# Kernel tuning notes

Measured on AMD Instinct MI355X. Metric: run time of the kernel, lower is better.

## Reference

```python
import jax, jax.numpy as jnp
import numpy as np

CLIP = 5.0  # clip_value from init


def setup_inputs() -> dict:
    key = jax.random.key(0)
    ks = jax.random.split(key, 6)
    B, T, I, H = 128, 1024, 256, 512
    s = 1.0 / np.sqrt(H)
    return {
        "x": jax.random.normal(ks[0], (B, T, I), dtype=jnp.float32),
        "h0": jax.random.normal(ks[1], (1, H), dtype=jnp.float32),
        "w_ih": jax.random.normal(ks[2], (3 * H, I), dtype=jnp.float32) * s,
        "w_hh": jax.random.normal(ks[3], (3 * H, H), dtype=jnp.float32) * s,
        "b_ih": jax.random.normal(ks[4], (3 * H,), dtype=jnp.float32) * s,
        "b_hh": jax.random.normal(ks[5], (3 * H,), dtype=jnp.float32) * s,
    }


def reference(x, h0, w_ih, w_hh, b_ih, b_hh):
    # x: [B, T, I], h0: [1, H]
    B = x.shape[0]
    h_init = jnp.tile(h0, (B, 1))  # [B, H]
    # Precompute all input projections in one big GEMM: [T, B, 3H]
    gi_all = jnp.einsum('bti,gi->tbg', x, w_ih) + b_ih

    def step(h, gi):
        gh = h @ w_hh.T + b_hh                      # [B, 3H]
        ir, iz, inn = jnp.split(gi, 3, axis=-1)
        hr, hz, hn = jnp.split(gh, 3, axis=-1)
        r = jax.nn.sigmoid(ir + hr)
        z = jax.nn.sigmoid(iz + hz)
        n = jnp.tanh(inn + r * hn)
        h_new = (1.0 - z) * n + z * h
        h_new = jnp.clip(h_new, -CLIP, CLIP)
        return h_new, h_new

    h_last, out = jax.lax.scan(step, h_init, gi_all)  # out: [T, B, H]
    output = jnp.transpose(out, (1, 0, 2))            # [B, T, H]
    return output, h_last
```

## Files before the change

kernel.cpp:

```cpp
#include <hip/hip_runtime.h>
#include <math.h>

#define T_SEQ 1024
#define B_SZ  128
#define I_SZ  256
#define H_SZ  512
#define G_SZ  1536

#define NBS   8
#define MB    16
#define NHS   16
#define HB    32
#define GB    96
#define NTHR  384
#define PGB   384

typedef _Float16 f16;
typedef _Float16 half8 __attribute__((ext_vector_type(8)));
typedef _Float16 f16x4 __attribute__((ext_vector_type(4)));
typedef float f32x4 __attribute__((ext_vector_type(4)));

__device__ __forceinline__ f32x4 load_f4_cohere_nw(const void* p) {
    f32x4 v;
    asm volatile("global_load_dwordx4 %0, %1, off sc0 sc1" : "=v"(v) : "v"(p));
    return v;
}
__device__ __forceinline__ f16x4 load_f16x4_nw(const void* p) {
    f16x4 v;
    asm volatile("global_load_dwordx2 %0, %1, off" : "=v"(v) : "v"(p));
    return v;
}
__device__ __forceinline__ unsigned load_u32_cohere(const void* p) {
    unsigned v;
    asm volatile("global_load_dword %0, %1, off sc0 sc1\n\ts_waitcnt vmcnt(0)"
                 : "=v"(v) : "v"(p) : "memory");
    return v;
}
__device__ __forceinline__ void store_u32_cohere(void* p, unsigned v) {
    asm volatile("global_store_dword %0, %1, off sc0 sc1"
                 :: "v"(p), "v"(v) : "memory");
}
__device__ __forceinline__ void wait_vm0() {
    asm volatile("s_waitcnt vmcnt(0)" ::: "memory");
    __builtin_amdgcn_sched_barrier(0);
}
__device__ __forceinline__ void wait_vm1() {
    asm volatile("s_waitcnt vmcnt(1)" ::: "memory");
    __builtin_amdgcn_sched_barrier(0);
}

__global__ void setup_kernel(const float* __restrict__ w_ih,
                             const float* __restrict__ w_hh,
                             const float* __restrict__ h0,
                             f16* __restrict__ wp16,
                             f16* __restrict__ wf16,
                             f16* __restrict__ hbuf0,
                             unsigned int* __restrict__ flags) {
    const int i0 = blockIdx.x * blockDim.x + threadIdx.x;
    const int stride = gridDim.x * blockDim.x;
    for (int i = i0; i < I_SZ * G_SZ; i += stride)
        wp16[i] = (f16)w_ih[i];
    for (int i = i0; i < NHS * GB * H_SZ; i += stride) {
        int hs  = i / (GB * H_SZ);
        int rem = i % (GB * H_SZ);
        int gl = rem / H_SZ, k = rem % H_SZ;
        int gate = gl >> 5, c = gl & 31;
        int gg = gate * H_SZ + hs * HB + c;
        wf16[i] = (f16)w_hh[(size_t)gg * H_SZ + k];
    }
    for (int i = i0; i < B_SZ * H_SZ; i += stride)
        hbuf0[i] = (f16)h0[i % H_SZ];
    if (i0 < NBS * NHS * 16) flags[i0] = 0;
}

__global__ __launch_bounds__(512, 1)
void proj_kernel(const float* __restrict__ x,
                 const f16* __restrict__ wp16,
                 const float* __restrict__ b_ih,
                 f16* __restrict__ gi16) {
    const int t  = blockIdx.x >> 2;
    const int g0 = (blockIdx.x & 3) * PGB;
    const int tid  = threadIdx.x;
    const int wid  = tid >> 6;
    const int lane = tid & 63;
    const int col  = lane & 15;
    const int krow = lane >> 4;

    __shared__ __align__(16) unsigned char x_lds[128 * 512];

    #pragma unroll
    for (int j = 0; j < 8; ++j) {
        int idx = tid + j * 512;
        int b = idx >> 5, k16 = idx & 31;
        const float* xp = x + ((size_t)b * T_SEQ + t) * I_SZ + k16 * 8;
        float4 v0 = *reinterpret_cast<const float4*>(xp);
        float4 v1 = *reinterpret_cast<const float4*>(xp + 4);
        half8 hv;
        hv[0] = (f16)v0.x; hv[1] = (f16)v0.y; hv[2] = (f16)v0.z; hv[3] = (f16)v0.w;
        hv[4] = (f16)v1.x; hv[5] = (f16)v1.y; hv[6] = (f16)v1.z; hv[7] = (f16)v1.w;
        unsigned addr = ((unsigned)(b * 512 + k16 * 16)) ^ (((unsigned)(b & 7)) << 4);
        *reinterpret_cast<half8*>(x_lds + addr) = hv;
    }

    const int gw0 = g0 + wid * 48;
    half8 af[3][8];
    #pragma unroll
    for (int m = 0; m < 3; ++m)
        #pragma unroll
        for (int k = 0; k < 8; ++k)
            af[m][k] = *reinterpret_cast<const half8*>(
                wp16 + (size_t)(gw0 + m * 16 + col) * I_SZ + k * 32 + krow * 8);

    float bias[3][4];
    #pragma unroll
    for (int m = 0; m < 3; ++m)
        #pragma unroll
        for (int r = 0; r < 4; ++r)
            bias[m][r] = b_ih[gw0 + m * 16 + krow * 4 + r];

    __syncthreads();

    #pragma unroll
    for (int nt = 0; nt < 8; ++nt) {
        const int b0 = nt * 16;
        f32x4 acc0 = {0.f,0.f,0.f,0.f}, acc1 = {0.f,0.f,0.f,0.f}, acc2 = {0.f,0.f,0.f,0.f};
        const int brow = b0 + col;
        const unsigned bswz = ((unsigned)(brow & 7)) << 4;
        #pragma unroll
        for (int k = 0; k < 8; ++k) {
            half8 bf = *reinterpret_cast<const half8*>(
                x_lds + (((unsigned)(brow * 512 + k * 64 + krow * 16)) ^ bswz));
            acc0 = __builtin_amdgcn_mfma_f32_16x16x32_f16(af[0][k], bf, acc0, 0, 0, 0);
            acc1 = __builtin_amdgcn_mfma_f32_16x16x32_f16(af[1][k], bf, acc1, 0, 0, 0);
            acc2 = __builtin_amdgcn_mfma_f32_16x16x32_f16(af[2][k], bf, acc2, 0, 0, 0);
        }
        #pragma unroll
        for (int r = 0; r < 4; ++r) {
            int gr = gw0 + krow * 4 + r;
            gi16[((size_t)t * G_SZ + gr)      * B_SZ + brow] = (f16)(acc0[r] + bias[0][r]);
            gi16[((size_t)t * G_SZ + gr + 16) * B_SZ + brow] = (f16)(acc1[r] + bias[1][r]);
            gi16[((size_t)t * G_SZ + gr + 32) * B_SZ + brow] = (f16)(acc2[r] + bias[2][r]);
        }
    }
}

__global__ __launch_bounds__(NTHR, 1)
void gru_persist(const f16* __restrict__ gi,
                 const f16* __restrict__ wf16,
                 const float* __restrict__ h0,
                 const float* __restrict__ b_hh,
                 f16* __restrict__ hbuf0,
                 f16* __restrict__ hbuf1,
                 unsigned int* __restrict__ flags,
                 float* __restrict__ out) {
    const int bs  = blockIdx.x & (NBS - 1);
    const int hs  = blockIdx.x >> 3;
    const int tid = threadIdx.x;

    __shared__ __align__(16) unsigned char h_lds[MB * H_SZ * 2];
    __shared__ float act_r[MB][HB + 1];
    __shared__ float act_z[MB][HB + 1];
    __shared__ float act_n[MB][HB + 1];
    __shared__ float act_i[MB][HB + 1];

    const int wid  = tid >> 6;
    const int lane = tid & 63;
    const int gate = wid >> 1;
    const int sub  = wid & 1;
    const int col  = lane & 15;
    const int krow = lane >> 4;
    const int c_local = sub * 16 + col;
    const int g_glob  = gate * H_SZ + hs * HB + c_local;

    half8 bfrag[16];
    {
        const f16* wp = wf16 + ((size_t)hs * GB + gate * HB + c_local) * H_SZ
                             + krow * 8;
        #pragma unroll
        for (int kk = 0; kk < 16; ++kk)
            bfrag[kk] = *reinterpret_cast<const half8*>(wp + kk * 32);
    }
    const float bias = b_hh[g_glob];

    const int cb = tid >> 4;
    const int cc = (tid & 15) * 2;
    float hm0 = 0.f, hm1 = 0.f;
    if (tid < 256) { hm0 = h0[hs * HB + cc]; hm1 = h0[hs * HB + cc + 1]; }

    const unsigned a_base = (unsigned)(col * 1024 + krow * 16);
    const unsigned a_swz  = ((unsigned)(col & 7)) << 4;

    unsigned int* myflag = flags + (size_t)(bs * NHS + hs) * 16;

    for (int t = 0; t < T_SEQ; ++t) {
        const f16* hin = (t & 1) ? hbuf1 : hbuf0;
        f16*      hout = (t & 1) ? hbuf0 : hbuf1;

        const int i0 = tid, i1 = tid + NTHR, i2 = tid + 2 * NTHR;
        f32x4 hv0 = load_f4_cohere_nw(
            hin + (size_t)(bs * MB + (i0 >> 6)) * H_SZ + (i0 & 63) * 8);
        f32x4 hv1 = load_f4_cohere_nw(
            hin + (size_t)(bs * MB + (i1 >> 6)) * H_SZ + (i1 & 63) * 8);
        f32x4 hv2;
        if (i2 < 1024)
            hv2 = load_f4_cohere_nw(
                hin + (size_t)(bs * MB + (i2 >> 6)) * H_SZ + (i2 & 63) * 8);
        f16x4 gv = load_f16x4_nw(
            gi + ((size_t)t * G_SZ + g_glob) * B_SZ + bs * MB + krow * 4);
        wait_vm1();

        {
            unsigned a0 = ((unsigned)((i0 >> 6) * 1024 + (i0 & 63) * 16))
                          ^ (((unsigned)((i0 >> 6) & 7)) << 4);
            *reinterpret_cast<f32x4*>(h_lds + a0) = hv0;
            unsigned a1 = ((unsigned)((i1 >> 6) * 1024 + (i1 & 63) * 16))
                          ^ (((unsigned)((i1 >> 6) & 7)) << 4);
            *reinterpret_cast<f32x4*>(h_lds + a1) = hv1;
            if (i2 < 1024) {
                unsigned a2 = ((unsigned)((i2 >> 6) * 1024 + (i2 & 63) * 16))
                              ^ (((unsigned)((i2 >> 6) & 7)) << 4);
                *reinterpret_cast<f32x4*>(h_lds + a2) = hv2;
            }
        }
        __syncthreads();

        f32x4 acc = {0.f, 0.f, 0.f, 0.f};
        #pragma unroll
        for (int kk = 0; kk < 16; ++kk) {
            half8 av = *reinterpret_cast<const half8*>(
                h_lds + ((a_base + kk * 64) ^ a_swz));
            acc = __builtin_amdgcn_mfma_f32_16x16x32_f16(av, bfrag[kk], acc, 0, 0, 0);
        }
        wait_vm0();

        if (gate == 0) {
            #pragma unroll
            for (int r = 0; r < 4; ++r)
                act_r[krow * 4 + r][c_local] =
                    1.f / (1.f + __expf(-(acc[r] + bias + (float)gv[r])));
        } else if (gate == 1) {
            #pragma unroll
            for (int r = 0; r < 4; ++r)
                act_z[krow * 4 + r][c_local] =
                    1.f / (1.f + __expf(-(acc[r] + bias + (float)gv[r])));
        } else {
            #pragma unroll
            for (int r = 0; r < 4; ++r) {
                act_n[krow * 4 + r][c_local] = acc[r] + bias;
                act_i[krow * 4 + r][c_local] = (float)gv[r];
            }
        }
        __syncthreads();

        if (tid < 256) {
            float r0 = act_r[cb][cc],     r1 = act_r[cb][cc + 1];
            float z0 = act_z[cb][cc],     z1 = act_z[cb][cc + 1];
            float a0 = act_i[cb][cc]     + r0 * act_n[cb][cc];
            float a1 = act_i[cb][cc + 1] + r1 * act_n[cb][cc + 1];
            float n0 = 1.f - 2.f / (__expf(2.f * a0) + 1.f);
            float n1 = 1.f - 2.f / (__expf(2.f * a1) + 1.f);
            float hn0 = (1.f - z0) * n0 + z0 * hm0;
            float hn1 = (1.f - z1) * n1 + z1 * hm1;
            hn0 = fminf(fmaxf(hn0, -5.f), 5.f);
            hn1 = fminf(fmaxf(hn1, -5.f), 5.f);
            hm0 = hn0; hm1 = hn1;

            const int bg = bs * MB + cb;
            const int hg = hs * HB + cc;

            f16 p0 = (f16)hn0, p1 = (f16)hn1;
            unsigned pack = (unsigned)__builtin_bit_cast(unsigned short, p0)
                          | ((unsigned)__builtin_bit_cast(unsigned short, p1) << 16);
            store_u32_cohere(hout + (size_t)bg * H_SZ + hg, pack);

            *reinterpret_cast<float2*>(
                out + ((size_t)bg * T_SEQ + t) * H_SZ + hg) = make_float2(hn0, hn1);

            if (t == T_SEQ - 1)
                *reinterpret_cast<float2*>(
                    out + (size_t)B_SZ * T_SEQ * H_SZ + (size_t)bg * H_SZ + hg) =
                    make_float2(hn0, hn1);
        }

        wait_vm1();
        __syncthreads();
        if (t < T_SEQ - 1) {
            if (tid == 0) store_u32_cohere(myflag, (unsigned)(t + 1));
            if (tid < 16) {
                const unsigned int* fp = flags + (size_t)(bs * NHS + tid) * 16;
                int guard = 0;
                unsigned v;
                do {
                    v = load_u32_cohere(fp);
                } while (__any(v < (unsigned)(t + 1)) && ++guard < (1 << 22));
            }
            __syncthreads();
        }
    }
}

extern "C" void kernel_launch(void* const* d_in, const int* in_sizes, int n_in,
                              void* d_out, int out_size, void* d_ws, size_t ws_size,
                              hipStream_t stream) {
    const float* x    = (const float*)d_in[0];
    const float* h0   = (const float*)d_in[1];
    const float* w_ih = (const float*)d_in[2];
    const float* w_hh = (const float*)d_in[3];
    const float* b_ih = (const float*)d_in[4];
    const float* b_hh = (const float*)d_in[5];
    float* out = (float*)d_out;

    char* p = (char*)d_ws;
    f16* wp16  = (f16*)p;                 p += (size_t)I_SZ * G_SZ * 2;
    f16* wf16  = (f16*)p;                 p += (size_t)NHS * GB * H_SZ * 2;
    f16* hbuf0 = (f16*)p;                 p += (size_t)B_SZ * H_SZ * 2;
    f16* hbuf1 = (f16*)p;                 p += (size_t)B_SZ * H_SZ * 2;
    unsigned int* flags = (unsigned int*)p; p += (size_t)NBS * NHS * 16 * 4;
    f16* gi = (f16*)p;

    setup_kernel<<<512, 256, 0, stream>>>(w_ih, w_hh, h0, wp16, wf16, hbuf0, flags);

    proj_kernel<<<T_SEQ * 4, 512, 0, stream>>>(x, wp16, b_ih, gi);

    gru_persist<<<NBS * NHS, NTHR, 0, stream>>>(gi, wf16, h0, b_hh,
                                                hbuf0, hbuf1, flags, out);
}
```

Before: 3.091 ms.

## Replace flag barrier with per-block sentinel mailboxes for hidden-state exchange

Drops the per-step flag store and spin barrier between workgroups. Each producer now broadcasts its packed hidden slice into a private double-buffered mailbox for every consumer block, and consumers poll the data itself until no sentinel value remains, then reset the slots to the sentinel. This removes a global synchronization round trip per timestep, at the cost of 16x more coherent stores per step and sentinel-based correctness, which depends on no real fp16 value matching the sentinel pattern. It also relays out the gi projections per batch slice and splits the MFMA accumulation into two independent chains.

```diff
diff --git a/kernel.cpp b/kernel.cpp
--- a/kernel.cpp
+++ b/kernel.cpp
@@ -15,38 +15,37 @@
 #define NTHR  384
 #define PGB   384
 
+#define SENT32 0x7FFF7FFFu
+
 typedef _Float16 f16;
 typedef _Float16 half8 __attribute__((ext_vector_type(8)));
 typedef _Float16 f16x4 __attribute__((ext_vector_type(4)));
 typedef float f32x4 __attribute__((ext_vector_type(4)));
-
-__device__ __forceinline__ f32x4 load_f4_cohere_nw(const void* p) {
+typedef unsigned uint32x4 __attribute__((ext_vector_type(4)));
+
+__device__ __forceinline__ f32x4 cload_f4(const void* p) {
     f32x4 v;
     asm volatile("global_load_dwordx4 %0, %1, off sc0 sc1" : "=v"(v) : "v"(p));
     return v;
+}
+__device__ __forceinline__ void cstore_f4(void* p, f32x4 v) {
+    asm volatile("global_store_dwordx4 %0, %1, off sc0 sc1" :: "v"(p), "v"(v) : "memory");
+}
+__device__ __forceinline__ void cstore_u32(void* p, unsigned v) {
+    asm volatile("global_store_dword %0, %1, off sc0 sc1" :: "v"(p), "v"(v) : "memory");
 }
 __device__ __forceinline__ f16x4 load_f16x4_nw(const void* p) {
     f16x4 v;
     asm volatile("global_load_dwordx2 %0, %1, off" : "=v"(v) : "v"(p));
     return v;
 }
-__device__ __forceinline__ unsigned load_u32_cohere(const void* p) {
-    unsigned v;
-    asm volatile("global_load_dword %0, %1, off sc0 sc1\n\ts_waitcnt vmcnt(0)"
-                 : "=v"(v) : "v"(p) : "memory");
-    return v;
-}
-__device__ __forceinline__ void store_u32_cohere(void* p, unsigned v) {
-    asm volatile("global_store_dword %0, %1, off sc0 sc1"
-                 :: "v"(p), "v"(v) : "memory");
-}
 __device__ __forceinline__ void wait_vm0() {
     asm volatile("s_waitcnt vmcnt(0)" ::: "memory");
     __builtin_amdgcn_sched_barrier(0);
 }
-__device__ __forceinline__ void wait_vm1() {
-    asm volatile("s_waitcnt vmcnt(1)" ::: "memory");
-    __builtin_amdgcn_sched_barrier(0);
+__device__ __forceinline__ bool stale4(f32x4 v) {
+    uint32x4 u = __builtin_bit_cast(uint32x4, v);
+    return (u[0] == SENT32) | (u[1] == SENT32) | (u[2] == SENT32) | (u[3] == SENT32);
 }
 
 __global__ void setup_kernel(const float* __restrict__ w_ih,
@@ -54,8 +53,7 @@
                              const float* __restrict__ h0,
                              f16* __restrict__ wp16,
                              f16* __restrict__ wf16,
-                             f16* __restrict__ hbuf0,
-                             unsigned int* __restrict__ flags) {
+                             f16* __restrict__ hbox) {
     const int i0 = blockIdx.x * blockDim.x + threadIdx.x;
     const int stride = gridDim.x * blockDim.x;
     for (int i = i0; i < I_SZ * G_SZ; i += stride)
@@ -68,9 +66,13 @@
         int gg = gate * H_SZ + hs * HB + c;
         wf16[i] = (f16)w_hh[(size_t)gg * H_SZ + k];
     }
-    for (int i = i0; i < B_SZ * H_SZ; i += stride)
-        hbuf0[i] = (f16)h0[i % H_SZ];
-    if (i0 < NBS * NHS * 16) flags[i0] = 0;
+    const int htot = 2 * NBS * NHS * MB * H_SZ;
+    const int half = htot / 2;
+    const f16 sent = __builtin_bit_cast(f16, (unsigned short)0x7FFF);
+    for (int i = i0; i < htot; i += stride) {
+        if (i < half) hbox[i] = (f16)h0[i & (H_SZ - 1)];
+        else          hbox[i] = sent;
+    }
 }
 
 __global__ __launch_bounds__(512, 1)
@@ -134,12 +136,14 @@
             acc1 = __builtin_amdgcn_mfma_f32_16x16x32_f16(af[1][k], bf, acc1, 0, 0, 0);
             acc2 = __builtin_amdgcn_mfma_f32_16x16x32_f16(af[2][k], bf, acc2, 0, 0, 0);
         }
+        const int pbs = brow >> 4;
+        const int pm  = brow & 15;
         #pragma unroll
         for (int r = 0; r < 4; ++r) {
             int gr = gw0 + krow * 4 + r;
-            gi16[((size_t)t * G_SZ + gr)      * B_SZ + brow] = (f16)(acc0[r] + bias[0][r]);
-            gi16[((size_t)t * G_SZ + gr + 16) * B_SZ + brow] = (f16)(acc1[r] + bias[1][r]);
-            gi16[((size_t)t * G_SZ + gr + 32) * B_SZ + brow] = (f16)(acc2[r] + bias[2][r]);
+            gi16[((size_t)(t * NBS + pbs) * G_SZ + gr)      * MB + pm] = (f16)(acc0[r] + bias[0][r]);
+            gi16[((size_t)(t * NBS + pbs) * G_SZ + gr + 16) * MB + pm] = (f16)(acc1[r] + bias[1][r]);
+            gi16[((size_t)(t * NBS + pbs) * G_SZ + gr + 32) * MB + pm] = (f16)(acc2[r] + bias[2][r]);
         }
     }
 }
@@ -149,9 +153,7 @@
                  const f16* __restrict__ wf16,
                  const float* __restrict__ h0,
                  const float* __restrict__ b_hh,
-                 f16* __restrict__ hbuf0,
-                 f16* __restrict__ hbuf1,
-                 unsigned int* __restrict__ flags,
+                 f16* __restrict__ hbox,
                  float* __restrict__ out) {
     const int bs  = blockIdx.x & (NBS - 1);
     const int hs  = blockIdx.x >> 3;
@@ -190,47 +192,71 @@
     const unsigned a_base = (unsigned)(col * 1024 + krow * 16);
     const unsigned a_swz  = ((unsigned)(col & 7)) << 4;
 
-    unsigned int* myflag = flags + (size_t)(bs * NHS + hs) * 16;
+    const size_t inbox_sz = (size_t)MB * H_SZ;
+    const int i0 = tid, i1 = tid + NTHR, i2 = tid + 2 * NTHR;
+    const bool has2 = (i2 < 1024);
+
+    const f32x4 sentv = __builtin_bit_cast(f32x4,
+        (uint32x4){SENT32, SENT32, SENT32, SENT32});
 
     for (int t = 0; t < T_SEQ; ++t) {
-        const f16* hin = (t & 1) ? hbuf1 : hbuf0;
-        f16*      hout = (t & 1) ? hbuf0 : hbuf1;
-
-        const int i0 = tid, i1 = tid + NTHR, i2 = tid + 2 * NTHR;
-        f32x4 hv0 = load_f4_cohere_nw(
-            hin + (size_t)(bs * MB + (i0 >> 6)) * H_SZ + (i0 & 63) * 8);
-        f32x4 hv1 = load_f4_cohere_nw(
-            hin + (size_t)(bs * MB + (i1 >> 6)) * H_SZ + (i1 & 63) * 8);
-        f32x4 hv2;
-        if (i2 < 1024)
-            hv2 = load_f4_cohere_nw(
-                hin + (size_t)(bs * MB + (i2 >> 6)) * H_SZ + (i2 & 63) * 8);
+        const int p  = t & 1;
+        const int p1 = p ^ 1;
+        f16* mybox = hbox + ((size_t)(p * NBS + bs) * NHS + hs) * inbox_sz;
+        f16* a0p = mybox + (i0 >> 6) * H_SZ + (i0 & 63) * 8;
+        f16* a1p = mybox + (i1 >> 6) * H_SZ + (i1 & 63) * 8;
+        f16* a2p = mybox + (i2 >> 6) * H_SZ + (i2 & 63) * 8;
+
         f16x4 gv = load_f16x4_nw(
-            gi + ((size_t)t * G_SZ + g_glob) * B_SZ + bs * MB + krow * 4);
-        wait_vm1();
-
+            gi + ((size_t)(t * NBS + bs) * G_SZ + g_glob) * MB + krow * 4);
+
+        f32x4 v0 = cload_f4(a0p);
+        f32x4 v1 = cload_f4(a1p);
+        f32x4 v2;
+        if (has2) v2 = cload_f4(a2p);
+        wait_vm0();
         {
-            unsigned a0 = ((unsigned)((i0 >> 6) * 1024 + (i0 & 63) * 16))
+            int guard = 0;
+            bool s0 = stale4(v0), s1 = stale4(v1), s2 = has2 && stale4(v2);
+            while (__any(s0 | s1 | s2)) {
+                if (s0) v0 = cload_f4(a0p);
+                if (s1) v1 = cload_f4(a1p);
+                if (s2) v2 = cload_f4(a2p);
+                wait_vm0();
+                s0 = stale4(v0); s1 = stale4(v1); s2 = has2 && stale4(v2);
+                if (++guard > 4096) break;
+            }
+        }
+
+        {
+            unsigned l0 = ((unsigned)((i0 >> 6) * 1024 + (i0 & 63) * 16))
                           ^ (((unsigned)((i0 >> 6) & 7)) << 4);
-            *reinterpret_cast<f32x4*>(h_lds + a0) = hv0;
-            unsigned a1 = ((unsigned)((i1 >> 6) * 1024 + (i1 & 63) * 16))
+            *reinterpret_cast<f32x4*>(h_lds + l0) = v0;
+            unsigned l1 = ((unsigned)((i1 >> 6) * 1024 + (i1 & 63) * 16))
                           ^ (((unsigned)((i1 >> 6) & 7)) << 4);
-            *reinterpret_cast<f32x4*>(h_lds + a1) = hv1;
-            if (i2 < 1024) {
-                unsigned a2 = ((unsigned)((i2 >> 6) * 1024 + (i2 & 63) * 16))
+            *reinterpret_cast<f32x4*>(h_lds + l1) = v1;
+            if (has2) {
+                unsigned l2 = ((unsigned)((i2 >> 6) * 1024 + (i2 & 63) * 16))
                               ^ (((unsigned)((i2 >> 6) & 7)) << 4);
-                *reinterpret_cast<f32x4*>(h_lds + a2) = hv2;
+                *reinterpret_cast<f32x4*>(h_lds + l2) = v2;
             }
+            cstore_f4(a0p, sentv);
+            cstore_f4(a1p, sentv);
+            if (has2) cstore_f4(a2p, sentv);
         }
         __syncthreads();
 
-        f32x4 acc = {0.f, 0.f, 0.f, 0.f};
-        #pragma unroll
-        for (int kk = 0; kk < 16; ++kk) {
-            half8 av = *reinterpret_cast<const half8*>(
-                h_lds + ((a_base + kk * 64) ^ a_swz));
-            acc = __builtin_amdgcn_mfma_f32_16x16x32_f16(av, bfrag[kk], acc, 0, 0, 0);
-        }
+        f32x4 accA = {0.f, 0.f, 0.f, 0.f}, accB = {0.f, 0.f, 0.f, 0.f};
+        #pragma unroll
+        for (int kk = 0; kk < 8; ++kk) {
+            half8 av0 = *reinterpret_cast<const half8*>(
+                h_lds + ((a_base + (2 * kk) * 64) ^ a_swz));
+            half8 av1 = *reinterpret_cast<const half8*>(
+                h_lds + ((a_base + (2 * kk + 1) * 64) ^ a_swz));
+            accA = __builtin_amdgcn_mfma_f32_16x16x32_f16(av0, bfrag[2 * kk],     accA, 0, 0, 0);
+            accB = __builtin_amdgcn_mfma_f32_16x16x32_f16(av1, bfrag[2 * kk + 1], accB, 0, 0, 0);
+        }
+        f32x4 acc = accA + accB;
         wait_vm0();
 
         if (gate == 0) {
@@ -268,10 +294,14 @@
             const int bg = bs * MB + cb;
             const int hg = hs * HB + cc;
 
-            f16 p0 = (f16)hn0, p1 = (f16)hn1;
-            unsigned pack = (unsigned)__builtin_bit_cast(unsigned short, p0)
-                          | ((unsigned)__builtin_bit_cast(unsigned short, p1) << 16);
-            store_u32_cohere(hout + (size_t)bg * H_SZ + hg, pack);
+            f16 q0 = (f16)hn0, q1 = (f16)hn1;
+            unsigned pack = (unsigned)__builtin_bit_cast(unsigned short, q0)
+                          | ((unsigned)__builtin_bit_cast(unsigned short, q1) << 16);
+            f16* wp = hbox + ((size_t)(p1 * NBS + bs) * NHS) * inbox_sz
+                           + (size_t)cb * H_SZ + hg;
+            #pragma unroll
+            for (int j = 0; j < NHS; ++j)
+                cstore_u32(wp + (size_t)j * inbox_sz, pack);
 
             *reinterpret_cast<float2*>(
                 out + ((size_t)bg * T_SEQ + t) * H_SZ + hg) = make_float2(hn0, hn1);
@@ -280,21 +310,6 @@
                 *reinterpret_cast<float2*>(
                     out + (size_t)B_SZ * T_SEQ * H_SZ + (size_t)bg * H_SZ + hg) =
                     make_float2(hn0, hn1);
-        }
-
-        wait_vm1();
-        __syncthreads();
-        if (t < T_SEQ - 1) {
-            if (tid == 0) store_u32_cohere(myflag, (unsigned)(t + 1));
-            if (tid < 16) {
-                const unsigned int* fp = flags + (size_t)(bs * NHS + tid) * 16;
-                int guard = 0;
-                unsigned v;
-                do {
-                    v = load_u32_cohere(fp);
-                } while (__any(v < (unsigned)(t + 1)) && ++guard < (1 << 22));
-            }
-            __syncthreads();
         }
     }
 }
@@ -311,17 +326,14 @@
     float* out = (float*)d_out;
 
     char* p = (char*)d_ws;
-    f16* wp16  = (f16*)p;                 p += (size_t)I_SZ * G_SZ * 2;
-    f16* wf16  = (f16*)p;                 p += (size_t)NHS * GB * H_SZ * 2;
-    f16* hbuf0 = (f16*)p;                 p += (size_t)B_SZ * H_SZ * 2;
-    f16* hbuf1 = (f16*)p;                 p += (size_t)B_SZ * H_SZ * 2;
-    unsigned int* flags = (unsigned int*)p; p += (size_t)NBS * NHS * 16 * 4;
-    f16* gi = (f16*)p;
-
-    setup_kernel<<<512, 256, 0, stream>>>(w_ih, w_hh, h0, wp16, wf16, hbuf0, flags);
+    f16* wp16 = (f16*)p;   p += (size_t)I_SZ * G_SZ * 2;
+    f16* wf16 = (f16*)p;   p += (size_t)NHS * GB * H_SZ * 2;
+    f16* hbox = (f16*)p;   p += (size_t)2 * NBS * NHS * MB * H_SZ * 2;
+    f16* gi   = (f16*)p;
+
+    setup_kernel<<<512, 256, 0, stream>>>(w_ih, w_hh, h0, wp16, wf16, hbox);
 
     proj_kernel<<<T_SEQ * 4, 512, 0, stream>>>(x, wp16, b_ih, gi);
 
-    gru_persist<<<NBS * NHS, NTHR, 0, stream>>>(gi, wf16, h0, b_hh,
-                                                hbuf0, hbuf1, flags, out);
-}
+    gru_persist<<<NBS * NHS, NTHR, 0, stream>>>(gi, wf16, h0, b_hh, hbox, out);
+}
```

Measured after the change: 4.371 ms. 41.4% more time.
